# Kernel tuning notes

Hardware: AMD Instinct MI355X
Metric: run time of the kernel (lower is better)

## Reference

```python
import jax, jax.numpy as jnp
import numpy as np

N, D, M, H, FF, L = 8192, 14, 36, 256, 2048, 2  # rows, d_model, material feats, mlp hidden, ffn, layers
EPS = 1e-5


def _ln(x, g, b):
    mu = jnp.mean(x, axis=-1, keepdims=True)
    var = jnp.mean((x - mu) ** 2, axis=-1, keepdims=True)
    return (x - mu) * jax.lax.rsqrt(var + EPS) * g + b


def setup_inputs() -> dict:
    key = jax.random.key(0)
    ks = iter(jax.random.split(key, 32))
    p = lambda shape, fan: jax.random.normal(next(ks), shape, jnp.float32) * (fan ** -0.5)
    return {
        "x": jax.random.normal(next(ks), (N, D), jnp.float32),
        "y": jax.random.normal(next(ks), (N, M), jnp.float32),
        # 2 post-LN TransformerEncoderLayers (nhead=1, dim_feedforward=2048, relu)
        "attn_wqkv": p((L, 3 * D, D), D), "attn_bqkv": p((L, 3 * D), D),
        "attn_wo": p((L, D, D), D), "attn_bo": p((L, D), D),
        "ln1_g": jnp.ones((L, D)), "ln1_b": jnp.zeros((L, D)),
        "ff_w1": p((L, FF, D), D), "ff_b1": p((L, FF), D),
        "ff_w2": p((L, D, FF), FF), "ff_b2": p((L, D), FF),
        "ln2_g": jnp.ones((L, D)), "ln2_b": jnp.zeros((L, D)),
        "fc1_w": p((D, D), D), "fc1_b": p((D,), D),
        "fc2_w": p((1, D), D), "fc2_b": p((1,), D),
        "fc3_w": p((H, D + M + 1), D + M + 1), "fc3_b": p((H,), D + M + 1),
        "fc4_w": p((H, H), H), "fc4_b": p((H,), H),
        "fc5_w": p((1, H), H), "fc5_b": p((1,), H),
    }


def reference(x, y, attn_wqkv, attn_bqkv, attn_wo, attn_bo, ln1_g, ln1_b,
              ff_w1, ff_b1, ff_w2, ff_b2, ln2_g, ln2_b,
              fc1_w, fc1_b, fc2_w, fc2_b, fc3_w, fc3_b, fc4_w, fc4_b, fc5_w, fc5_b):
    h = x  # [N, D]; batch of size 1 squeezed away
    for l in range(L):
        qkv = h @ attn_wqkv[l].T + attn_bqkv[l]            # [N, 3D]
        q, k, v = jnp.split(qkv, 3, axis=-1)
        scores = (q @ k.T) * (D ** -0.5)                   # [N, N]
        a = jax.nn.softmax(scores, axis=-1) @ v            # [N, D]
        a = a @ attn_wo[l].T + attn_bo[l]
        h = _ln(h + a, ln1_g[l], ln1_b[l])
        f = jax.nn.relu(h @ ff_w1[l].T + ff_b1[l]) @ ff_w2[l].T + ff_b2[l]
        h = _ln(h + f, ln2_g[l], ln2_b[l])
    x1 = h @ fc1_w.T + fc1_b                               # [N, D]
    size_out = (x1 @ fc2_w.T + fc2_b)[:, 0]                # [N]

    # batched replacement of the per-row python loop
    size_int = size_out.astype(jnp.int32)                  # trunc toward zero, like .int()
    size_f = size_int.astype(jnp.float32)[:, None]         # [N, 1]
    reg_in = jnp.concatenate([size_f, x, y], axis=1)       # [N, 1+D+M]
    r = jax.nn.relu(reg_in @ fc3_w.T + fc3_b)
    r = jax.nn.relu(r @ fc4_w.T + fc4_b)
    reg_values = (r @ fc5_w.T + fc5_b)[:, 0]               # [N]
    reg_values = jnp.where(size_int != 0, reg_values, 0.0)
    return size_out, reg_values
```

## Files before the change

### kernel.cpp

```cpp
#include <hip/hip_runtime.h>
#include <math.h>

#define NN 8192
#define DD 14
#define DP 16
#define FF 2048
#define HID 256
#define LN_EPS 1e-5f
#define NCH 16
#define NFCH 8
#define QSCALE (1.4426950408889634f / 3.7416573867739413f)

typedef short bf16x8 __attribute__((ext_vector_type(8)));
typedef float f32x4 __attribute__((ext_vector_type(4)));

#define LOAD16(dst, srcp) { \
  const float4* _p = (const float4*)(srcp); \
  float4 _a = _p[0], _b = _p[1], _c = _p[2], _d = _p[3]; \
  dst[0]=_a.x; dst[1]=_a.y; dst[2]=_a.z; dst[3]=_a.w; \
  dst[4]=_b.x; dst[5]=_b.y; dst[6]=_b.z; dst[7]=_b.w; \
  dst[8]=_c.x; dst[9]=_c.y; dst[10]=_c.z; dst[11]=_c.w; \
  dst[12]=_d.x; dst[13]=_d.y; dst[14]=_d.z; dst[15]=_d.w; }

#define STORE16(dstp, src) { \
  float4* _p = (float4*)(dstp); \
  _p[0] = make_float4(src[0], src[1], src[2], src[3]); \
  _p[1] = make_float4(src[4], src[5], src[6], src[7]); \
  _p[2] = make_float4(src[8], src[9], src[10], src[11]); \
  _p[3] = make_float4(src[12], src[13], src[14], src[15]); }

static __device__ __forceinline__ float fast_exp2(float x) {
#if __has_builtin(__builtin_amdgcn_exp2f)
  return __builtin_amdgcn_exp2f(x);
#else
  return exp2f(x);
#endif
}

static __device__ __forceinline__ unsigned short bf_hi(float x) {
  return (unsigned short)(__float_as_uint(x) >> 16);
}
static __device__ __forceinline__ float bf_hi_f(float x) {
  return __uint_as_float(__float_as_uint(x) & 0xffff0000u);
}

static __device__ __forceinline__ void split8(const float* pv, bf16x8* ph, bf16x8* pl) {
  #pragma unroll
  for (int i = 0; i < 8; i++) {
    unsigned int u = __float_as_uint(pv[i]);
    (*ph)[i] = (short)(u >> 16);
    float rr = pv[i] - __uint_as_float(u & 0xffff0000u);
    (*pl)[i] = (short)(__float_as_uint(rr) >> 16);
  }
}

static __device__ __forceinline__ void qkv_compute_store(
    int r, const float* hr, const float* __restrict__ wqkv,
    const float* __restrict__ bqkv, unsigned int* __restrict__ Qpack,
    unsigned int* __restrict__ KB1, unsigned int* __restrict__ KB2,
    unsigned short* __restrict__ VhiT, unsigned short* __restrict__ VloT) {
  float q[14], k[14], v[14];
  #pragma unroll 6
  for (int c = 0; c < 42; c++) {
    const float* w = wqkv + c * 14;
    float s = bqkv[c];
    #pragma unroll
    for (int d = 0; d < 14; d++) s = fmaf(hr[d], w[d], s);
    if (c < 14)       q[c] = s * QSCALE;
    else if (c < 28)  k[c - 14] = s;
    else              v[c - 28] = s;
  }
  unsigned int qp[16], k1[16], k2[16];
  unsigned short qh[14], ql[14], kh[14], kl[14];
  #pragma unroll
  for (int d = 0; d < 14; d++) {
    qh[d] = bf_hi(q[d]);
    ql[d] = bf_hi(q[d] - bf_hi_f(q[d]));
    kh[d] = bf_hi(k[d]);
    kl[d] = bf_hi(k[d] - bf_hi_f(k[d]));
  }
  #pragma unroll
  for (int i = 0; i < 7; i++) {
    qp[i]     = (unsigned int)qh[2*i] | ((unsigned int)qh[2*i+1] << 16);
    qp[8 + i] = (unsigned int)ql[2*i] | ((unsigned int)ql[2*i+1] << 16);
    k1[i]     = (unsigned int)kh[2*i] | ((unsigned int)kh[2*i+1] << 16);
    k1[8 + i] = k1[i];
    k2[i]     = (unsigned int)kl[2*i] | ((unsigned int)kl[2*i+1] << 16);
    k2[8 + i] = k2[i];
  }
  qp[7] = 0; qp[15] = 0; k1[7] = 0; k1[15] = 0; k2[7] = 0; k2[15] = 0;
  uint4* Qp4 = (uint4*)(Qpack + (size_t)r * 16);
  uint4* K14 = (uint4*)(KB1 + (size_t)r * 16);
  uint4* K24 = (uint4*)(KB2 + (size_t)r * 16);
  #pragma unroll
  for (int i = 0; i < 4; i++) {
    Qp4[i] = make_uint4(qp[4*i], qp[4*i+1], qp[4*i+2], qp[4*i+3]);
    K14[i] = make_uint4(k1[4*i], k1[4*i+1], k1[4*i+2], k1[4*i+3]);
    K24[i] = make_uint4(k2[4*i], k2[4*i+1], k2[4*i+2], k2[4*i+3]);
  }
  #pragma unroll
  for (int d = 0; d < 14; d++) {
    VhiT[(size_t)d * NN + r] = bf_hi(v[d]);
    VloT[(size_t)d * NN + r] = bf_hi(v[d] - bf_hi_f(v[d]));
  }
  VhiT[(size_t)14 * NN + r] = 0x3F80;
  VhiT[(size_t)15 * NN + r] = 0;
  VloT[(size_t)14 * NN + r] = 0;
  VloT[(size_t)15 * NN + r] = 0;
}

static __device__ __forceinline__ void store_apack(unsigned int* dst, const float* o) {
  unsigned int qp[16];
  unsigned short hh[14], ll[14];
  #pragma unroll
  for (int d = 0; d < 14; d++) {
    hh[d] = bf_hi(o[d]);
    ll[d] = bf_hi(o[d] - bf_hi_f(o[d]));
  }
  #pragma unroll
  for (int i = 0; i < 7; i++) {
    qp[i]     = (unsigned int)hh[2*i] | ((unsigned int)hh[2*i+1] << 16);
    qp[8 + i] = (unsigned int)ll[2*i] | ((unsigned int)ll[2*i+1] << 16);
  }
  qp[7] = 0; qp[15] = 0;
  uint4* d4 = (uint4*)dst;
  #pragma unroll
  for (int i = 0; i < 4; i++)
    d4[i] = make_uint4(qp[4*i], qp[4*i+1], qp[4*i+2], qp[4*i+3]);
}

__global__ void pack_all(const float* __restrict__ w3, const float* __restrict__ w4,
                         const float* __restrict__ ffw1, const float* __restrict__ ffw2,
                         const float* __restrict__ x, const float* __restrict__ wqkv,
                         const float* __restrict__ bqkv, float* __restrict__ h,
                         unsigned int* __restrict__ Qpack,
                         unsigned int* __restrict__ KB1, unsigned int* __restrict__ KB2,
                         unsigned short* __restrict__ VhiT, unsigned short* __restrict__ VloT,
                         unsigned short* __restrict__ B3h, unsigned short* __restrict__ B3l,
                         unsigned short* __restrict__ B4h, unsigned short* __restrict__ B4l,
                         unsigned int* __restrict__ W1B1, unsigned int* __restrict__ W1B2,
                         unsigned short* __restrict__ W2h, unsigned short* __restrict__ W2l) {
  const int blk = blockIdx.x, tid = threadIdx.x;
  if (blk < 32) {
    int t = blk * 256 + tid;
    int lane = t & 63, ks = (t >> 6) & 7, nt = t >> 9;
    int n = nt * 16 + (lane & 15);
    int k0 = ks * 32 + (lane >> 4) * 8;
    unsigned int h4[4], l4[4];
    #pragma unroll
    for (int jj = 0; jj < 4; jj++) {
      unsigned short h2[2], l2[2];
      #pragma unroll
      for (int e = 0; e < 2; e++) {
        float v = w4[(size_t)n * 256 + k0 + jj * 2 + e];
        h2[e] = bf_hi(v);
        l2[e] = bf_hi(v - bf_hi_f(v));
      }
      h4[jj] = (unsigned int)h2[0] | ((unsigned int)h2[1] << 16);
      l4[jj] = (unsigned int)l2[0] | ((unsigned int)l2[1] << 16);
    }
    ((uint4*)B4h)[t] = make_uint4(h4[0], h4[1], h4[2], h4[3]);
    ((uint4*)B4l)[t] = make_uint4(l4[0], l4[1], l4[2], l4[3]);
    if (ks < 2) {
      int fi = (nt * 2 + ks) * 64 + lane;
      #pragma unroll
      for (int jj = 0; jj < 4; jj++) {
        unsigned short h2[2], l2[2];
        #pragma unroll
        for (int e = 0; e < 2; e++) {
          int k = k0 + jj * 2 + e;
          float v = (k < 51) ? w3[(size_t)n * 51 + k] : 0.f;
          h2[e] = bf_hi(v);
          l2[e] = bf_hi(v - bf_hi_f(v));
        }
        h4[jj] = (unsigned int)h2[0] | ((unsigned int)h2[1] << 16);
        l4[jj] = (unsigned int)l2[0] | ((unsigned int)l2[1] << 16);
      }
      ((uint4*)B3h)[fi] = make_uint4(h4[0], h4[1], h4[2], h4[3]);
      ((uint4*)B3l)[fi] = make_uint4(l4[0], l4[1], l4[2], l4[3]);
    }
  } else if (blk < 48) {
    int t = (blk - 32) * 256 + tid;
    int l = t >> 11, j = t & 2047;
    const float* wrow = ffw1 + ((size_t)l * FF + j) * 14;
    unsigned int k1[16], k2[16];
    unsigned short kh[14], kl[14];
    #pragma unroll
    for (int d = 0; d < 14; d++) {
      float v = wrow[d];
      kh[d] = bf_hi(v);
      kl[d] = bf_hi(v - bf_hi_f(v));
    }
    #pragma unroll
    for (int i = 0; i < 7; i++) {
      k1[i] = (unsigned int)kh[2*i] | ((unsigned int)kh[2*i+1] << 16);
      k1[8 + i] = k1[i];
      k2[i] = (unsigned int)kl[2*i] | ((unsigned int)kl[2*i+1] << 16);
      k2[8 + i] = k2[i];
    }
    k1[7] = 0; k1[15] = 0; k2[7] = 0; k2[15] = 0;
    uint4* d1 = (uint4*)(W1B1 + (size_t)t * 16);
    uint4* d2 = (uint4*)(W1B2 + (size_t)t * 16);
    #pragma unroll
    for (int i = 0; i < 4; i++) {
      d1[i] = make_uint4(k1[4*i], k1[4*i+1], k1[4*i+2], k1[4*i+3]);
      d2[i] = make_uint4(k2[4*i], k2[4*i+1], k2[4*i+2], k2[4*i+3]);
    }
  } else if (blk < 64) {
    int t = (blk - 48) * 256 + tid;
    int l = t >> 11, j = t & 2047;
    #pragma unroll
    for (int d = 0; d < 16; d++) {
      float v = (d < 14) ? ffw2[((size_t)l * 14 + d) * FF + j] : 0.f;
      W2h[((size_t)l * 16 + d) * FF + j] = bf_hi(v);
      W2l[((size_t)l * 16 + d) * FF + j] = bf_hi(v - bf_hi_f(v));
    }
  } else {
    int r = (blk - 64) * 256 + tid;
    float hr[16];
    #pragma unroll
    for (int d = 0; d < 14; d++) hr[d] = x[(size_t)r * 14 + d];
    hr[14] = 0.f; hr[15] = 0.f;
    STORE16(h + (size_t)r * DP, hr);
    qkv_compute_store(r, hr, wqkv, bqkv, Qpack, KB1, KB2, VhiT, VloT);
  }
}

__global__ __launch_bounds__(256, 4) void attn_mfma(
    const unsigned int* __restrict__ Qpack, const unsigned int* __restrict__ KB1,
    const unsigned int* __restrict__ KB2, const unsigned short* __restrict__ VhiT,
    const unsigned short* __restrict__ VloT, float* __restrict__ part) {
  __shared__ float Plds[4][32][36];
  const int tid = threadIdx.x;
  const int wave = tid >> 6;
  const int lane = tid & 63;
  const int lo4 = lane & 15;
  const int hi4 = lane >> 4;
  const int qbase = blockIdx.x * 128 + wave * 32;
  const int kbase0 = blockIdx.y * 512;

  const bf16x8* Qp = (const bf16x8*)Qpack;
  const bf16x8* B1 = (const bf16x8*)KB1;
  const bf16x8* B2 = (const bf16x8*)KB2;
  const bf16x8* Vh = (const bf16x8*)VhiT;
  const bf16x8* Vl = (const bf16x8*)VloT;

  bf16x8 aQ0 = Qp[(size_t)(qbase + lo4) * 4 + hi4];
  bf16x8 aQ1 = Qp[(size_t)(qbase + 16 + lo4) * 4 + hi4];
  f32x4 acc0 = {0.f, 0.f, 0.f, 0.f};
  f32x4 acc1 = {0.f, 0.f, 0.f, 0.f};
  const f32x4 zero = {0.f, 0.f, 0.f, 0.f};

  for (int c = 0; c < 16; c++) {
    const int kb = kbase0 + c * 32;
    bf16x8 b1g0 = B1[(size_t)(kb + lo4) * 4 + hi4];
    bf16x8 b2g0 = B2[(size_t)(kb + lo4) * 4 + hi4];
    bf16x8 b1g1 = B1[(size_t)(kb + 16 + lo4) * 4 + hi4];
    bf16x8 b2g1 = B2[(size_t)(kb + 16 + lo4) * 4 + hi4];
    bf16x8 vh = Vh[(size_t)lo4 * 1024 + (kb >> 3) + hi4];
    bf16x8 vl = Vl[(size_t)lo4 * 1024 + (kb >> 3) + hi4];

    f32x4 s00 = __builtin_amdgcn_mfma_f32_16x16x32_bf16(aQ0, b1g0, zero, 0, 0, 0);
    f32x4 s01 = __builtin_amdgcn_mfma_f32_16x16x32_bf16(aQ0, b1g1, zero, 0, 0, 0);
    f32x4 s10 = __builtin_amdgcn_mfma_f32_16x16x32_bf16(aQ1, b1g0, zero, 0, 0, 0);
    f32x4 s11 = __builtin_amdgcn_mfma_f32_16x16x32_bf16(aQ1, b1g1, zero, 0, 0, 0);
    s00 = __builtin_amdgcn_mfma_f32_16x16x32_bf16(aQ0, b2g0, s00, 0, 0, 0);
    s01 = __builtin_amdgcn_mfma_f32_16x16x32_bf16(aQ0, b2g1, s01, 0, 0, 0);
    s10 = __builtin_amdgcn_mfma_f32_16x16x32_bf16(aQ1, b2g0, s10, 0, 0, 0);
    s11 = __builtin_amdgcn_mfma_f32_16x16x32_bf16(aQ1, b2g1, s11, 0, 0, 0);
    #pragma unroll
    for (int reg = 0; reg < 4; reg++) {
      Plds[wave][hi4 * 4 + reg][lo4]           = fast_exp2(s00[reg]);
      Plds[wave][hi4 * 4 + reg][16 + lo4]      = fast_exp2(s01[reg]);
      Plds[wave][16 + hi4 * 4 + reg][lo4]      = fast_exp2(s10[reg]);
      Plds[wave][16 + hi4 * 4 + reg][16 + lo4] = fast_exp2(s11[reg]);
    }
    __asm__ volatile("s_waitcnt lgkmcnt(0)" ::: "memory");
    const float4* p0 = (const float4*)&Plds[wave][lo4][hi4 * 8];
    const float4* p1 = (const float4*)&Plds[wave][16 + lo4][hi4 * 8];
    float4 a0 = p0[0], a1 = p0[1], c0 = p1[0], c1 = p1[1];
    float pv0[8] = {a0.x, a0.y, a0.z, a0.w, a1.x, a1.y, a1.z, a1.w};
    float pv1[8] = {c0.x, c0.y, c0.z, c0.w, c1.x, c1.y, c1.z, c1.w};
// ... 205 lines not shown
    const float* __restrict__ h, const float* __restrict__ part,
    const float* __restrict__ b2, const float* __restrict__ g, const float* __restrict__ b,
    const float* __restrict__ fc1w, const float* __restrict__ fc1b,
    const float* __restrict__ fc2w, const float* __restrict__ fc2b,
    const float* __restrict__ x, const float* __restrict__ y,
    const unsigned short* __restrict__ B3h, const unsigned short* __restrict__ B3l,
    const float* __restrict__ b3,
    const unsigned short* __restrict__ B4h, const unsigned short* __restrict__ B4l,
    const float* __restrict__ b4,
    const float* __restrict__ w5, const float* __restrict__ b5,
    float* __restrict__ out, float* __restrict__ outr) {
  __shared__ alignas(16) unsigned short Ah[16][72], Al[16][72];
  __shared__ alignas(16) unsigned short R1h[16][264], R1l[16][264];
  __shared__ float sred[4][16][16];
  __shared__ float szf[16];
  const int tid = threadIdx.x;
  const int wave = tid >> 6;
  const int lane = tid & 63;
  const int lo4 = lane & 15;
  const int hi4 = lane >> 4;
  const int rbase = blockIdx.x * 16;

  if (tid < 128) {
    int m = tid >> 3, c = tid & 7;
    int r = rbase + m;
    float p[16];
    LOAD16(p, part + ((size_t)c * NN + r) * 16);
    float f[14];
    #pragma unroll
    for (int d = 0; d < 14; d++) f[d] = p[d];
    #pragma unroll
    for (int off = 1; off < 8; off <<= 1) {
      #pragma unroll
      for (int d = 0; d < 14; d++) f[d] += __shfl_xor(f[d], off, 64);
    }
    if (c == 0) {
      float hr[16];
      LOAD16(hr, h + (size_t)r * DP);
      float xx[14];
      #pragma unroll
      for (int i = 0; i < 14; i++) xx[i] = hr[i] + f[i] + b2[i];
      float mu = 0.f;
      #pragma unroll
      for (int i = 0; i < 14; i++) mu += xx[i];
      mu *= (1.f / 14.f);
      float var = 0.f;
      #pragma unroll
      for (int i = 0; i < 14; i++) { float tt = xx[i] - mu; var = fmaf(tt, tt, var); }
      var *= (1.f / 14.f);
      float rs = rsqrtf(var + LN_EPS);
      float o[14];
      #pragma unroll
      for (int i = 0; i < 14; i++) o[i] = fmaf((xx[i] - mu) * rs, g[i], b[i]);
      float s = fc2b[0];
      #pragma unroll
      for (int i = 0; i < 14; i++) {
        float tt = fc1b[i];
        #pragma unroll
        for (int d = 0; d < 14; d++) tt = fmaf(fc1w[i * 14 + d], o[d], tt);
        s = fmaf(tt, fc2w[i], s);
      }
      out[r] = s;
      int si = (int)s;
      szf[m] = (float)si;
    }
  }
  __syncthreads();

  for (int idx = tid; idx < 16 * 64; idx += 256) {
    int m = idx >> 6, k = idx & 63;
    int r = rbase + m;
    float v = 0.f;
    if (k == 0)       v = szf[m];
    else if (k < 15)  v = x[(size_t)r * 14 + (k - 1)];
    else if (k < 51)  v = y[(size_t)r * 36 + (k - 15)];
    Ah[m][k] = bf_hi(v);
    Al[m][k] = bf_hi(v - bf_hi_f(v));
  }
  __syncthreads();

  const f32x4 zero = {0.f, 0.f, 0.f, 0.f};
  f32x4 acc[4];
  #pragma unroll
  for (int nt = 0; nt < 4; nt++) acc[nt] = zero;

  #pragma unroll
  for (int ks = 0; ks < 2; ks++) {
    bf16x8 ah = *(const bf16x8*)&Ah[lo4][ks * 32 + hi4 * 8];
    bf16x8 al = *(const bf16x8*)&Al[lo4][ks * 32 + hi4 * 8];
    #pragma unroll
    for (int nt = 0; nt < 4; nt++) {
      int fi = ((wave * 4 + nt) * 2 + ks) * 64 + lane;
      bf16x8 bh = ((const bf16x8*)B3h)[fi];
      bf16x8 bl = ((const bf16x8*)B3l)[fi];
      acc[nt] = __builtin_amdgcn_mfma_f32_16x16x32_bf16(ah, bh, acc[nt], 0, 0, 0);
      acc[nt] = __builtin_amdgcn_mfma_f32_16x16x32_bf16(al, bh, acc[nt], 0, 0, 0);
      acc[nt] = __builtin_amdgcn_mfma_f32_16x16x32_bf16(ah, bl, acc[nt], 0, 0, 0);
    }
  }
  #pragma unroll
  for (int nt = 0; nt < 4; nt++) {
    int n = (wave * 4 + nt) * 16 + lo4;
    float bb = b3[n];
    #pragma unroll
    for (int reg = 0; reg < 4; reg++) {
      int m = hi4 * 4 + reg;
      float v = fmaxf(acc[nt][reg] + bb, 0.f);
      R1h[m][n] = bf_hi(v);
      R1l[m][n] = bf_hi(v - bf_hi_f(v));
    }
  }
  __syncthreads();

  #pragma unroll
  for (int nt = 0; nt < 4; nt++) acc[nt] = zero;
  #pragma unroll
  for (int ks = 0; ks < 8; ks++) {
    bf16x8 ah = *(const bf16x8*)&R1h[lo4][ks * 32 + hi4 * 8];
    bf16x8 al = *(const bf16x8*)&R1l[lo4][ks * 32 + hi4 * 8];
    #pragma unroll
    for (int nt = 0; nt < 4; nt++) {
      int fi = ((wave * 4 + nt) * 8 + ks) * 64 + lane;
      bf16x8 bh = ((const bf16x8*)B4h)[fi];
      bf16x8 bl = ((const bf16x8*)B4l)[fi];
      acc[nt] = __builtin_amdgcn_mfma_f32_16x16x32_bf16(ah, bh, acc[nt], 0, 0, 0);
      acc[nt] = __builtin_amdgcn_mfma_f32_16x16x32_bf16(al, bh, acc[nt], 0, 0, 0);
      acc[nt] = __builtin_amdgcn_mfma_f32_16x16x32_bf16(ah, bl, acc[nt], 0, 0, 0);
    }
  }
  float s[4] = {0.f, 0.f, 0.f, 0.f};
  #pragma unroll
  for (int nt = 0; nt < 4; nt++) {
    int n = (wave * 4 + nt) * 16 + lo4;
    float bb = b4[n], ww = w5[n];
    #pragma unroll
    for (int reg = 0; reg < 4; reg++)
      s[reg] = fmaf(fmaxf(acc[nt][reg] + bb, 0.f), ww, s[reg]);
  }
  #pragma unroll
  for (int reg = 0; reg < 4; reg++) sred[wave][hi4 * 4 + reg][lo4] = s[reg];
  __syncthreads();

  if (tid < 16) {
    float t = b5[0];
    #pragma unroll
    for (int w = 0; w < 4; w++) {
      const float4* p = (const float4*)&sred[w][tid][0];
      float4 a0 = p[0], a1 = p[1], a2 = p[2], a3 = p[3];
      t += ((a0.x + a0.y) + (a0.z + a0.w)) + ((a1.x + a1.y) + (a1.z + a1.w)) +
           ((a2.x + a2.y) + (a2.z + a2.w)) + ((a3.x + a3.y) + (a3.z + a3.w));
    }
    float sz = szf[tid];
    outr[rbase + tid] = (sz != 0.f) ? t : 0.f;
  }
}

extern "C" void kernel_launch(void* const* d_in, const int* in_sizes, int n_in,
                              void* d_out, int out_size, void* d_ws, size_t ws_size,
                              hipStream_t stream) {
  const float* x    = (const float*)d_in[0];
  const float* y    = (const float*)d_in[1];
  const float* wqkv = (const float*)d_in[2];
  const float* bqkv = (const float*)d_in[3];
  const float* wo   = (const float*)d_in[4];
  const float* bo   = (const float*)d_in[5];
  const float* ln1g = (const float*)d_in[6];
  const float* ln1b = (const float*)d_in[7];
  const float* ffw1 = (const float*)d_in[8];
  const float* ffb1 = (const float*)d_in[9];
  const float* ffw2 = (const float*)d_in[10];
  const float* ffb2 = (const float*)d_in[11];
  const float* ln2g = (const float*)d_in[12];
  const float* ln2b = (const float*)d_in[13];
  const float* fc1w = (const float*)d_in[14];
  const float* fc1b = (const float*)d_in[15];
  const float* fc2w = (const float*)d_in[16];
  const float* fc2b = (const float*)d_in[17];
  const float* fc3w = (const float*)d_in[18];
  const float* fc3b = (const float*)d_in[19];
  const float* fc4w = (const float*)d_in[20];
  const float* fc4b = (const float*)d_in[21];
  const float* fc5w = (const float*)d_in[22];
  const float* fc5b = (const float*)d_in[23];

  float* ws = (float*)d_ws;
  float*          h     = ws;
  unsigned int*   Qpack = (unsigned int*)(ws + 131072);
  unsigned int*   KB1   = (unsigned int*)(ws + 262144);
  unsigned int*   KB2   = (unsigned int*)(ws + 393216);
  unsigned short* VhiT  = (unsigned short*)(ws + 524288);
  unsigned short* VloT  = (unsigned short*)(ws + 589824);
  unsigned int*   Hpack = (unsigned int*)(ws + 655360);
  float*          part  = ws + 786432;
  unsigned short* B3h   = (unsigned short*)(ws + 2891776);
  unsigned short* B3l   = (unsigned short*)(ws + 2899968);
  unsigned short* B4h   = (unsigned short*)(ws + 2908160);
  unsigned short* B4l   = (unsigned short*)(ws + 2940928);
  unsigned int*   W1B1  = (unsigned int*)(ws + 2973696);
  unsigned int*   W1B2  = (unsigned int*)(ws + 3039232);
  unsigned short* W2h   = (unsigned short*)(ws + 3104768);
  unsigned short* W2l   = (unsigned short*)(ws + 3137536);

  float* out = (float*)d_out;

  pack_all<<<96, 256, 0, stream>>>(fc3w, fc4w, ffw1, ffw2, x, wqkv, bqkv, h,
                                   Qpack, KB1, KB2, VhiT, VloT,
                                   B3h, B3l, B4h, B4l, W1B1, W1B2, W2h, W2l);
  for (int l = 0; l < 2; l++) {
    attn_mfma<<<dim3(64, NCH), 256, 0, stream>>>(Qpack, KB1, KB2, VhiT, VloT, part);
    attn_comb_ln1<<<256, 128, 0, stream>>>(h, part, wo + (size_t)l * 196,
                                           bo + (size_t)l * 14, ln1g + (size_t)l * 14,
                                           ln1b + (size_t)l * 14, Hpack);
    ffn_mfma<<<dim3(64, NFCH), 256, 0, stream>>>(
        Hpack, W1B1 + (size_t)l * 2048 * 16, W1B2 + (size_t)l * 2048 * 16,
        W2h + (size_t)l * 16 * FF, W2l + (size_t)l * 16 * FF,
        ffb1 + (size_t)l * FF, part);
    if (l == 0) {
      ffn_ln2_qkv<<<256, 128, 0, stream>>>(h, part, ffb2, ln2g, ln2b,
                                           wqkv + 42 * 14, bqkv + 42,
                                           Qpack, KB1, KB2, VhiT, VloT);
    }
  }
  tail_fused<<<512, 256, 0, stream>>>(h, part, ffb2 + 14, ln2g + 14, ln2b + 14,
                                      fc1w, fc1b, fc2w, fc2b, x, y,
                                      B3h, B3l, fc3b, B4h, B4l, fc4b,
                                      fc5w, fc5b, out, out + NN);
}
```

Baseline: 258.5 us.

## Fuse all pipeline stages into one persistent cooperative kernel with grid syncs

Replaces the sequence of nine kernel launches (packing, attention, combine+LN, FFN, LN+QKV, tail) with a single persistent cooperative kernel that loops over virtual blocks and separates stages with grid-wide syncs. The goal is to remove per-launch overhead and inter-kernel gaps on a short pipeline. In exchange, every stage runs at a fixed grid size capped by occupancy, and it pays grid.sync costs. If the cooperative launch fails, it falls back to the old multi-kernel path.

```diff
diff --git a/kernel.cpp b/kernel.cpp
--- a/kernel.cpp
+++ b/kernel.cpp
@@ -1,5 +1,8 @@
 #include <hip/hip_runtime.h>
+#include <hip/hip_cooperative_groups.h>
 #include <math.h>
+
+namespace cg = cooperative_groups;
 
 #define NN 8192
 #define DD 14
@@ -128,6 +131,7 @@
   for (int i = 0; i < 4; i++)
     d4[i] = make_uint4(qp[4*i], qp[4*i+1], qp[4*i+2], qp[4*i+3]);
 }
+
 
 __global__ void pack_all(const float* __restrict__ w3, const float* __restrict__ w4,
                          const float* __restrict__ ffw1, const float* __restrict__ ffw2,
@@ -639,6 +643,518 @@
     }
     float sz = szf[tid];
     outr[rbase + tid] = (sz != 0.f) ? t : 0.f;
+  }
+}
+
+
+struct P26 {
+  const float *x, *y, *wqkv, *bqkv, *wo, *bo, *ln1g, *ln1b;
+  const float *ffw1, *ffb1, *ffw2, *ffb2, *ln2g, *ln2b;
+  const float *fc1w, *fc1b, *fc2w, *fc2b, *fc3w, *fc3b, *fc4w, *fc4b, *fc5w, *fc5b;
+  float* ws;
+  float* out;
+};
+
+__global__ __launch_bounds__(256, 4) void fused_pipeline(P26 p) {
+  cg::grid_group grid = cg::this_grid();
+  __shared__ __attribute__((aligned(16))) char smem[25664];
+  const int tid = threadIdx.x;
+  const int wave = tid >> 6;
+  const int lane = tid & 63;
+  const int lo4 = lane & 15;
+  const int hi4 = lane >> 4;
+
+  float* ws = p.ws;
+  float*          h     = ws;
+  unsigned int*   Qpack = (unsigned int*)(ws + 131072);
+  unsigned int*   KB1   = (unsigned int*)(ws + 262144);
+  unsigned int*   KB2   = (unsigned int*)(ws + 393216);
+  unsigned short* VhiT  = (unsigned short*)(ws + 524288);
+  unsigned short* VloT  = (unsigned short*)(ws + 589824);
+  unsigned int*   Hpack = (unsigned int*)(ws + 655360);
+  float*          part  = ws + 786432;
+  unsigned short* B3h   = (unsigned short*)(ws + 2891776);
+  unsigned short* B3l   = (unsigned short*)(ws + 2899968);
+  unsigned short* B4h   = (unsigned short*)(ws + 2908160);
+  unsigned short* B4l   = (unsigned short*)(ws + 2940928);
+  unsigned int*   W1B1  = (unsigned int*)(ws + 2973696);
+  unsigned int*   W1B2  = (unsigned int*)(ws + 3039232);
+  unsigned short* W2h   = (unsigned short*)(ws + 3104768);
+  unsigned short* W2l   = (unsigned short*)(ws + 3137536);
+  float* out  = p.out;
+  float* outr = p.out + NN;
+
+  for (int vb = blockIdx.x; vb < 96; vb += gridDim.x) {
+    if (vb < 32) {
+      int t = vb * 256 + tid;
+      int ln = t & 63, ks = (t >> 6) & 7, nt = t >> 9;
+      int n = nt * 16 + (ln & 15);
+      int k0 = ks * 32 + (ln >> 4) * 8;
+      unsigned int h4[4], l4[4];
+      #pragma unroll
+      for (int jj = 0; jj < 4; jj++) {
+        unsigned short h2[2], l2[2];
+        #pragma unroll
+        for (int e = 0; e < 2; e++) {
+          float v = p.fc4w[(size_t)n * 256 + k0 + jj * 2 + e];
+          h2[e] = bf_hi(v);
+          l2[e] = bf_hi(v - bf_hi_f(v));
+        }
+        h4[jj] = (unsigned int)h2[0] | ((unsigned int)h2[1] << 16);
+        l4[jj] = (unsigned int)l2[0] | ((unsigned int)l2[1] << 16);
+      }
+      ((uint4*)B4h)[t] = make_uint4(h4[0], h4[1], h4[2], h4[3]);
+      ((uint4*)B4l)[t] = make_uint4(l4[0], l4[1], l4[2], l4[3]);
+      if (ks < 2) {
+        int fi = (nt * 2 + ks) * 64 + ln;
+        #pragma unroll
+        for (int jj = 0; jj < 4; jj++) {
+          unsigned short h2[2], l2[2];
+          #pragma unroll
+          for (int e = 0; e < 2; e++) {
+            int k = k0 + jj * 2 + e;
+            float v = (k < 51) ? p.fc3w[(size_t)n * 51 + k] : 0.f;
+            h2[e] = bf_hi(v);
+            l2[e] = bf_hi(v - bf_hi_f(v));
+          }
+          h4[jj] = (unsigned int)h2[0] | ((unsigned int)h2[1] << 16);
+          l4[jj] = (unsigned int)l2[0] | ((unsigned int)l2[1] << 16);
+        }
+        ((uint4*)B3h)[fi] = make_uint4(h4[0], h4[1], h4[2], h4[3]);
+        ((uint4*)B3l)[fi] = make_uint4(l4[0], l4[1], l4[2], l4[3]);
+      }
+    } else if (vb < 48) {
+      int t = (vb - 32) * 256 + tid;
+      int lw = t >> 11, j = t & 2047;
+      const float* wrow = p.ffw1 + ((size_t)lw * FF + j) * 14;
+      unsigned int k1[16], k2[16];
+      unsigned short kh[14], kl[14];
+      #pragma unroll
+      for (int d = 0; d < 14; d++) {
+        float v = wrow[d];
+        kh[d] = bf_hi(v);
+        kl[d] = bf_hi(v - bf_hi_f(v));
+      }
+      #pragma unroll
+      for (int i = 0; i < 7; i++) {
+        k1[i] = (unsigned int)kh[2*i] | ((unsigned int)kh[2*i+1] << 16);
+        k1[8 + i] = k1[i];
+        k2[i] = (unsigned int)kl[2*i] | ((unsigned int)kl[2*i+1] << 16);
+        k2[8 + i] = k2[i];
+      }
+      k1[7] = 0; k1[15] = 0; k2[7] = 0; k2[15] = 0;
+      uint4* d1 = (uint4*)(W1B1 + (size_t)t * 16);
+      uint4* d2 = (uint4*)(W1B2 + (size_t)t * 16);
+      #pragma unroll
+      for (int i = 0; i < 4; i++) {
+        d1[i] = make_uint4(k1[4*i], k1[4*i+1], k1[4*i+2], k1[4*i+3]);
+        d2[i] = make_uint4(k2[4*i], k2[4*i+1], k2[4*i+2], k2[4*i+3]);
+      }
+    } else if (vb < 64) {
+      int t = (vb - 48) * 256 + tid;
+      int lw = t >> 11, j = t & 2047;
+      #pragma unroll
+      for (int d = 0; d < 16; d++) {
+        float v = (d < 14) ? p.ffw2[((size_t)lw * 14 + d) * FF + j] : 0.f;
+        W2h[((size_t)lw * 16 + d) * FF + j] = bf_hi(v);
+        W2l[((size_t)lw * 16 + d) * FF + j] = bf_hi(v - bf_hi_f(v));
+      }
+    } else {
+      int r = (vb - 64) * 256 + tid;
+      float hr[16];
+      #pragma unroll
+      for (int d = 0; d < 14; d++) hr[d] = p.x[(size_t)r * 14 + d];
+      hr[14] = 0.f; hr[15] = 0.f;
+      STORE16(h + (size_t)r * DP, hr);
+      qkv_compute_store(r, hr, p.wqkv, p.bqkv, Qpack, KB1, KB2, VhiT, VloT);
+    }
+  }
+  grid.sync();
+
+  const bf16x8* Qp  = (const bf16x8*)Qpack;
+  const bf16x8* Kb1 = (const bf16x8*)KB1;
+  const bf16x8* Kb2 = (const bf16x8*)KB2;
+  const bf16x8* Vh  = (const bf16x8*)VhiT;
+  const bf16x8* Vl  = (const bf16x8*)VloT;
+  const bf16x8* Hp  = (const bf16x8*)Hpack;
+  const f32x4 zero = {0.f, 0.f, 0.f, 0.f};
+
+  for (int l = 0; l < 2; l++) {
+    for (int vb = blockIdx.x; vb < 1024; vb += gridDim.x) {
+      float (*Pl)[36] = reinterpret_cast<float(*)[36]>(smem + wave * 4608);
+      const int qbase = (vb & 63) * 128 + wave * 32;
+      const int kbase0 = (vb >> 6) * 512;
+      bf16x8 aQ0 = Qp[(size_t)(qbase + lo4) * 4 + hi4];
+      bf16x8 aQ1 = Qp[(size_t)(qbase + 16 + lo4) * 4 + hi4];
+      f32x4 acc0 = zero, acc1 = zero;
+      for (int c = 0; c < 16; c++) {
+        const int kb = kbase0 + c * 32;
+        bf16x8 b1g0 = Kb1[(size_t)(kb + lo4) * 4 + hi4];
+        bf16x8 b2g0 = Kb2[(size_t)(kb + lo4) * 4 + hi4];
+        bf16x8 b1g1 = Kb1[(size_t)(kb + 16 + lo4) * 4 + hi4];
+        bf16x8 b2g1 = Kb2[(size_t)(kb + 16 + lo4) * 4 + hi4];
+        bf16x8 vh = Vh[(size_t)lo4 * 1024 + (kb >> 3) + hi4];
+        bf16x8 vl = Vl[(size_t)lo4 * 1024 + (kb >> 3) + hi4];
+
+        f32x4 s00 = __builtin_amdgcn_mfma_f32_16x16x32_bf16(aQ0, b1g0, zero, 0, 0, 0);
+        f32x4 s01 = __builtin_amdgcn_mfma_f32_16x16x32_bf16(aQ0, b1g1, zero, 0, 0, 0);
+        f32x4 s10 = __builtin_amdgcn_mfma_f32_16x16x32_bf16(aQ1, b1g0, zero, 0, 0, 0);
+        f32x4 s11 = __builtin_amdgcn_mfma_f32_16x16x32_bf16(aQ1, b1g1, zero, 0, 0, 0);
+        s00 = __builtin_amdgcn_mfma_f32_16x16x32_bf16(aQ0, b2g0, s00, 0, 0, 0);
+        s01 = __builtin_amdgcn_mfma_f32_16x16x32_bf16(aQ0, b2g1, s01, 0, 0, 0);
+        s10 = __builtin_amdgcn_mfma_f32_16x16x32_bf16(aQ1, b2g0, s10, 0, 0, 0);
+        s11 = __builtin_amdgcn_mfma_f32_16x16x32_bf16(aQ1, b2g1, s11, 0, 0, 0);
+        #pragma unroll
+        for (int reg = 0; reg < 4; reg++) {
+          Pl[hi4 * 4 + reg][lo4]           = fast_exp2(s00[reg]);
+          Pl[hi4 * 4 + reg][16 + lo4]      = fast_exp2(s01[reg]);
+          Pl[16 + hi4 * 4 + reg][lo4]      = fast_exp2(s10[reg]);
+          Pl[16 + hi4 * 4 + reg][16 + lo4] = fast_exp2(s11[reg]);
+        }
+        __asm__ volatile("s_waitcnt lgkmcnt(0)" ::: "memory");
+        const float4* p0 = (const float4*)&Pl[lo4][hi4 * 8];
+        const float4* p1 = (const float4*)&Pl[16 + lo4][hi4 * 8];
+        float4 a0 = p0[0], a1 = p0[1], c0 = p1[0], c1 = p1[1];
+        float pv0[8] = {a0.x, a0.y, a0.z, a0.w, a1.x, a1.y, a1.z, a1.w};
+        float pv1[8] = {c0.x, c0.y, c0.z, c0.w, c1.x, c1.y, c1.z, c1.w};
+        bf16x8 ph0, pl0, ph1, pl1;
+        split8(pv0, &ph0, &pl0);
+        split8(pv1, &ph1, &pl1);
+        acc0 = __builtin_amdgcn_mfma_f32_16x16x32_bf16(ph0, vh, acc0, 0, 0, 0);
+        acc1 = __builtin_amdgcn_mfma_f32_16x16x32_bf16(ph1, vh, acc1, 0, 0, 0);
+        acc0 = __builtin_amdgcn_mfma_f32_16x16x32_bf16(pl0, vh, acc0, 0, 0, 0);
+        acc1 = __builtin_amdgcn_mfma_f32_16x16x32_bf16(pl1, vh, acc1, 0, 0, 0);
+        acc0 = __builtin_amdgcn_mfma_f32_16x16x32_bf16(ph0, vl, acc0, 0, 0, 0);
+        acc1 = __builtin_amdgcn_mfma_f32_16x16x32_bf16(ph1, vl, acc1, 0, 0, 0);
+        __asm__ volatile("s_waitcnt lgkmcnt(0)" ::: "memory");
+      }
+      float* pbase = part + (size_t)(vb >> 6) * NN * 16;
+      #pragma unroll
+      for (int reg = 0; reg < 4; reg++) {
+        int row0 = qbase + hi4 * 4 + reg;
+        pbase[(size_t)row0 * 16 + lo4] = acc0[reg];
+        pbase[(size_t)(row0 + 16) * 16 + lo4] = acc1[reg];
+      }
+    }
+    grid.sync();
+
+    {
+      const float* wol = p.wo + (size_t)l * 196;
+      const float* bol = p.bo + (size_t)l * 14;
+      const float* g1  = p.ln1g + (size_t)l * 14;
+      const float* bl1 = p.ln1b + (size_t)l * 14;
+      for (int vb = blockIdx.x; vb < 1024; vb += gridDim.x) {
+        int t = vb * 256 + tid;
+        int r = t >> 5, q = t & 31;
+        float L = 0.f;
+        float A[14];
+        #pragma unroll
+        for (int d = 0; d < 14; d++) A[d] = 0.f;
+        if (q < 16) {
+          float pp[16];
+          LOAD16(pp, part + ((size_t)q * NN + r) * 16);
+          L = pp[14];
+          #pragma unroll
+          for (int d = 0; d < 14; d++) A[d] = pp[d];
+        }
+        #pragma unroll
+        for (int off = 1; off < 16; off <<= 1) {
+          L += __shfl_xor(L, off, 64);
+          #pragma unroll
+          for (int d = 0; d < 14; d++) A[d] += __shfl_xor(A[d], off, 64);
+        }
+        if (q == 0) {
+          float inv = 1.f / L;
+          float a[14];
+          #pragma unroll
+          for (int d = 0; d < 14; d++) a[d] = A[d] * inv;
+          float hr[16];
+          LOAD16(hr, h + (size_t)r * DP);
+          float xx[14];
+          #pragma unroll
+          for (int i = 0; i < 14; i++) {
+            float s = bol[i];
+            #pragma unroll
+            for (int d = 0; d < 14; d++) s = fmaf(wol[i * 14 + d], a[d], s);
+            xx[i] = hr[i] + s;
+          }
+          float mu = 0.f;
+          #pragma unroll
+          for (int i = 0; i < 14; i++) mu += xx[i];
+          mu *= (1.f / 14.f);
+          float var = 0.f;
+          #pragma unroll
+          for (int i = 0; i < 14; i++) { float tt = xx[i] - mu; var = fmaf(tt, tt, var); }
+          var *= (1.f / 14.f);
+          float rs = rsqrtf(var + LN_EPS);
+          float o[16];
+          #pragma unroll
+          for (int i = 0; i < 14; i++) o[i] = fmaf((xx[i] - mu) * rs, g1[i], bl1[i]);
+          o[14] = 0.f; o[15] = 0.f;
+          STORE16(h + (size_t)r * DP, o);
+          store_apack(Hpack + (size_t)r * 16, o);
+        }
+      }
+    }
+    grid.sync();
+
+    {
+      const bf16x8* Wb1 = (const bf16x8*)(W1B1 + (size_t)l * 2048 * 16);
+      const bf16x8* Wb2 = (const bf16x8*)(W1B2 + (size_t)l * 2048 * 16);
+      const bf16x8* Wvh = (const bf16x8*)(W2h + (size_t)l * 16 * FF);
+      const bf16x8* Wvl = (const bf16x8*)(W2l + (size_t)l * 16 * FF);
+      const float* fb1 = p.ffb1 + (size_t)l * FF;
+      for (int vb = blockIdx.x; vb < 1024; vb += gridDim.x) {
+        float (*Pl)[36] = reinterpret_cast<float(*)[36]>(smem + wave * 4608);
+        const int qbase = (vb & 63) * 128 + wave * 32;
+        const int jbase0 = (vb >> 6) * 128;
+        bf16x8 aH0 = Hp[(size_t)(qbase + lo4) * 4 + hi4];
+        bf16x8 aH1 = Hp[(size_t)(qbase + 16 + lo4) * 4 + hi4];
+        f32x4 acc0 = zero, acc1 = zero;
+        for (int c = 0; c < 4; c++) {
+          const int jb = jbase0 + c * 32;
+          bf16x8 b1g0 = Wb1[(size_t)(jb + lo4) * 4 + hi4];
+          bf16x8 b2g0 = Wb2[(size_t)(jb + lo4) * 4 + hi4];
+          bf16x8 b1g1 = Wb1[(size_t)(jb + 16 + lo4) * 4 + hi4];
+          bf16x8 b2g1 = Wb2[(size_t)(jb + 16 + lo4) * 4 + hi4];
+          bf16x8 vh = Wvh[(size_t)lo4 * 256 + (jb >> 3) + hi4];
+          bf16x8 vl = Wvl[(size_t)lo4 * 256 + (jb >> 3) + hi4];
+          float bb0 = fb1[jb + lo4];
+          float bb1 = fb1[jb + 16 + lo4];
+
+          f32x4 s00 = __builtin_amdgcn_mfma_f32_16x16x32_bf16(aH0, b1g0, zero, 0, 0, 0);
+          f32x4 s01 = __builtin_amdgcn_mfma_f32_16x16x32_bf16(aH0, b1g1, zero, 0, 0, 0);
+          f32x4 s10 = __builtin_amdgcn_mfma_f32_16x16x32_bf16(aH1, b1g0, zero, 0, 0, 0);
+          f32x4 s11 = __builtin_amdgcn_mfma_f32_16x16x32_bf16(aH1, b1g1, zero, 0, 0, 0);
+          s00 = __builtin_amdgcn_mfma_f32_16x16x32_bf16(aH0, b2g0, s00, 0, 0, 0);
+          s01 = __builtin_amdgcn_mfma_f32_16x16x32_bf16(aH0, b2g1, s01, 0, 0, 0);
+          s10 = __builtin_amdgcn_mfma_f32_16x16x32_bf16(aH1, b2g0, s10, 0, 0, 0);
+          s11 = __builtin_amdgcn_mfma_f32_16x16x32_bf16(aH1, b2g1, s11, 0, 0, 0);
+          #pragma unroll
+          for (int reg = 0; reg < 4; reg++) {
+            Pl[hi4 * 4 + reg][lo4]           = fmaxf(s00[reg] + bb0, 0.f);
+            Pl[hi4 * 4 + reg][16 + lo4]      = fmaxf(s01[reg] + bb1, 0.f);
+            Pl[16 + hi4 * 4 + reg][lo4]      = fmaxf(s10[reg] + bb0, 0.f);
+            Pl[16 + hi4 * 4 + reg][16 + lo4] = fmaxf(s11[reg] + bb1, 0.f);
+          }
+          __asm__ volatile("s_waitcnt lgkmcnt(0)" ::: "memory");
+          const float4* p0 = (const float4*)&Pl[lo4][hi4 * 8];
+          const float4* p1 = (const float4*)&Pl[16 + lo4][hi4 * 8];
+          float4 a0 = p0[0], a1 = p0[1], c0 = p1[0], c1 = p1[1];
+          float pv0[8] = {a0.x, a0.y, a0.z, a0.w, a1.x, a1.y, a1.z, a1.w};
+          float pv1[8] = {c0.x, c0.y, c0.z, c0.w, c1.x, c1.y, c1.z, c1.w};
+          bf16x8 th0, tl0, th1, tl1;
+          split8(pv0, &th0, &tl0);
+          split8(pv1, &th1, &tl1);
+          acc0 = __builtin_amdgcn_mfma_f32_16x16x32_bf16(th0, vh, acc0, 0, 0, 0);
+          acc1 = __builtin_amdgcn_mfma_f32_16x16x32_bf16(th1, vh, acc1, 0, 0, 0);
+          acc0 = __builtin_amdgcn_mfma_f32_16x16x32_bf16(tl0, vh, acc0, 0, 0, 0);
+          acc1 = __builtin_amdgcn_mfma_f32_16x16x32_bf16(tl1, vh, acc1, 0, 0, 0);
+          acc0 = __builtin_amdgcn_mfma_f32_16x16x32_bf16(th0, vl, acc0, 0, 0, 0);
+          acc1 = __builtin_amdgcn_mfma_f32_16x16x32_bf16(th1, vl, acc1, 0, 0, 0);
+          __asm__ volatile("s_waitcnt lgkmcnt(0)" ::: "memory");
+        }
+        float* pbase = part + (size_t)(vb >> 6) * NN * 16;
+        #pragma unroll
+        for (int reg = 0; reg < 4; reg++) {
+          int row0 = qbase + hi4 * 4 + reg;
+          pbase[(size_t)row0 * 16 + lo4] = acc0[reg];
+          pbase[(size_t)(row0 + 16) * 16 + lo4] = acc1[reg];
+        }
+      }
+    }
+    grid.sync();
+
+    if (l == 0) {
+      for (int vb = blockIdx.x; vb < 1024; vb += gridDim.x) {
+        int t = vb * 256 + tid;
+        int r = t >> 5, q = t & 31;
+        float f[14];
+        #pragma unroll
+        for (int d = 0; d < 14; d++) f[d] = 0.f;
+        if (q < 16) {
+          float pp[16];
+          LOAD16(pp, part + ((size_t)q * NN + r) * 16);
+          #pragma unroll
+          for (int d = 0; d < 14; d++) f[d] = pp[d];
+        }
+        #pragma unroll
+        for (int off = 1; off < 16; off <<= 1) {
+          #pragma unroll
+          for (int d = 0; d < 14; d++) f[d] += __shfl_xor(f[d], off, 64);
+        }
+        if (q == 0) {
+          float hr[16];
+          LOAD16(hr, h + (size_t)r * DP);
+          float xx[14];
+          #pragma unroll
+          for (int i = 0; i < 14; i++) xx[i] = hr[i] + f[i] + p.ffb2[i];
+          float mu = 0.f;
+          #pragma unroll
+          for (int i = 0; i < 14; i++) mu += xx[i];
+          mu *= (1.f / 14.f);
+          float var = 0.f;
+          #pragma unroll
+          for (int i = 0; i < 14; i++) { float tt = xx[i] - mu; var = fmaf(tt, tt, var); }
+          var *= (1.f / 14.f);
+          float rs = rsqrtf(var + LN_EPS);
+          float o[16];
+          #pragma unroll
+          for (int i = 0; i < 14; i++) o[i] = fmaf((xx[i] - mu) * rs, p.ln2g[i], p.ln2b[i]);
+          o[14] = 0.f; o[15] = 0.f;
+          STORE16(h + (size_t)r * DP, o);
+          qkv_compute_store(r, o, p.wqkv + 588, p.bqkv + 42, Qpack, KB1, KB2, VhiT, VloT);
+        }
+      }
+      grid.sync();
+    }
+  }
+
+  {
+    unsigned short (*Ah)[72]  = (unsigned short(*)[72])(smem);
+    unsigned short (*Al)[72]  = (unsigned short(*)[72])(smem + 2304);
+    unsigned short (*R1h)[264] = (unsigned short(*)[264])(smem + 4608);
+    unsigned short (*R1l)[264] = (unsigned short(*)[264])(smem + 13056);
+    float (*sred)[16][16] = (float(*)[16][16])(smem + 21504);
+    float* szf = (float*)(smem + 25600);
+    const float* b2t = p.ffb2 + 14;
+    const float* g2t = p.ln2g + 14;
+    const float* bb2t = p.ln2b + 14;
+
+    for (int vb = blockIdx.x; vb < 512; vb += gridDim.x) {
+      const int rbase = vb * 16;
+      {
+        int m = tid >> 4, c = tid & 15;
+        int r = rbase + m;
+        float pp[16];
+        LOAD16(pp, part + ((size_t)c * NN + r) * 16);
+        float f[14];
+        #pragma unroll
+        for (int d = 0; d < 14; d++) f[d] = pp[d];
+        #pragma unroll
+        for (int off = 1; off < 16; off <<= 1) {
+          #pragma unroll
+          for (int d = 0; d < 14; d++) f[d] += __shfl_xor(f[d], off, 64);
+        }
+        if (c == 0) {
+          float hr[16];
+          LOAD16(hr, h + (size_t)r * DP);
+          float xx[14];
+          #pragma unroll
+          for (int i = 0; i < 14; i++) xx[i] = hr[i] + f[i] + b2t[i];
+          float mu = 0.f;
+          #pragma unroll
+          for (int i = 0; i < 14; i++) mu += xx[i];
+          mu *= (1.f / 14.f);
+          float var = 0.f;
+          #pragma unroll
+          for (int i = 0; i < 14; i++) { float tt = xx[i] - mu; var = fmaf(tt, tt, var); }
+          var *= (1.f / 14.f);
+          float rs = rsqrtf(var + LN_EPS);
+          float o[14];
+          #pragma unroll
+          for (int i = 0; i < 14; i++) o[i] = fmaf((xx[i] - mu) * rs, g2t[i], bb2t[i]);
+          float s = p.fc2b[0];
+          #pragma unroll
+          for (int i = 0; i < 14; i++) {
+            float tt = p.fc1b[i];
+            #pragma unroll
+            for (int d = 0; d < 14; d++) tt = fmaf(p.fc1w[i * 14 + d], o[d], tt);
+            s = fmaf(tt, p.fc2w[i], s);
+          }
+          out[r] = s;
+          int si = (int)s;
+          szf[m] = (float)si;
+        }
+      }
+      __syncthreads();
+
+      for (int idx = tid; idx < 16 * 64; idx += 256) {
+        int m = idx >> 6, k = idx & 63;
+        int r = rbase + m;
+        float v = 0.f;
+        if (k == 0)       v = szf[m];
+        else if (k < 15)  v = p.x[(size_t)r * 14 + (k - 1)];
+        else if (k < 51)  v = p.y[(size_t)r * 36 + (k - 15)];
+        Ah[m][k] = bf_hi(v);
+        Al[m][k] = bf_hi(v - bf_hi_f(v));
+      }
+      __syncthreads();
+
+      f32x4 acc[4];
+      #pragma unroll
+      for (int nt = 0; nt < 4; nt++) acc[nt] = zero;
+      #pragma unroll
+      for (int ks = 0; ks < 2; ks++) {
+        bf16x8 ah = *(const bf16x8*)&Ah[lo4][ks * 32 + hi4 * 8];
+        bf16x8 al = *(const bf16x8*)&Al[lo4][ks * 32 + hi4 * 8];
+        #pragma unroll
+        for (int nt = 0; nt < 4; nt++) {
+          int fi = ((wave * 4 + nt) * 2 + ks) * 64 + lane;
+          bf16x8 bh = ((const bf16x8*)B3h)[fi];
+          bf16x8 bl = ((const bf16x8*)B3l)[fi];
+          acc[nt] = __builtin_amdgcn_mfma_f32_16x16x32_bf16(ah, bh, acc[nt], 0, 0, 0);
+          acc[nt] = __builtin_amdgcn_mfma_f32_16x16x32_bf16(al, bh, acc[nt], 0, 0, 0);
+          acc[nt] = __builtin_amdgcn_mfma_f32_16x16x32_bf16(ah, bl, acc[nt], 0, 0, 0);
+        }
+      }
+      #pragma unroll
+      for (int nt = 0; nt < 4; nt++) {
+        int n = (wave * 4 + nt) * 16 + lo4;
+        float bb = p.fc3b[n];
+        #pragma unroll
+        for (int reg = 0; reg < 4; reg++) {
+          int m = hi4 * 4 + reg;
+          float v = fmaxf(acc[nt][reg] + bb, 0.f);
+          R1h[m][n] = bf_hi(v);
+          R1l[m][n] = bf_hi(v - bf_hi_f(v));
+        }
+      }
+      __syncthreads();
+
+      #pragma unroll
+      for (int nt = 0; nt < 4; nt++) acc[nt] = zero;
+      #pragma unroll
+      for (int ks = 0; ks < 8; ks++) {
+        bf16x8 ah = *(const bf16x8*)&R1h[lo4][ks * 32 + hi4 * 8];
+        bf16x8 al = *(const bf16x8*)&R1l[lo4][ks * 32 + hi4 * 8];
+        #pragma unroll
+        for (int nt = 0; nt < 4; nt++) {
+          int fi = ((wave * 4 + nt) * 8 + ks) * 64 + lane;
+          bf16x8 bh = ((const bf16x8*)B4h)[fi];
+          bf16x8 bl = ((const bf16x8*)B4l)[fi];
+          acc[nt] = __builtin_amdgcn_mfma_f32_16x16x32_bf16(ah, bh, acc[nt], 0, 0, 0);
+          acc[nt] = __builtin_amdgcn_mfma_f32_16x16x32_bf16(al, bh, acc[nt], 0, 0, 0);
+          acc[nt] = __builtin_amdgcn_mfma_f32_16x16x32_bf16(ah, bl, acc[nt], 0, 0, 0);
+        }
+      }
+      float s4[4] = {0.f, 0.f, 0.f, 0.f};
+      #pragma unroll
+      for (int nt = 0; nt < 4; nt++) {
+        int n = (wave * 4 + nt) * 16 + lo4;
+        float bb = p.fc4b[n], ww = p.fc5w[n];
+        #pragma unroll
+        for (int reg = 0; reg < 4; reg++)
+          s4[reg] = fmaf(fmaxf(acc[nt][reg] + bb, 0.f), ww, s4[reg]);
+      }
+      #pragma unroll
+      for (int reg = 0; reg < 4; reg++) sred[wave][hi4 * 4 + reg][lo4] = s4[reg];
+      __syncthreads();
+
+      if (tid < 16) {
+        float tsum = p.fc5b[0];
+        #pragma unroll
+        for (int w = 0; w < 4; w++) {
+          const float4* pr = (const float4*)&sred[w][tid][0];
+          float4 a0 = pr[0], a1 = pr[1], a2 = pr[2], a3 = pr[3];
+          tsum += ((a0.x + a0.y) + (a0.z + a0.w)) + ((a1.x + a1.y) + (a1.z + a1.w)) +
+                  ((a2.x + a2.y) + (a2.z + a2.w)) + ((a3.x + a3.y) + (a3.z + a3.w));
+        }
+        float sz = szf[tid];
+        outr[rbase + tid] = (sz != 0.f) ? tsum : 0.f;
+      }
+      __syncthreads();
+    }
   }
 }
 
@@ -690,26 +1206,53 @@
 
   float* out = (float*)d_out;
 
-  pack_all<<<96, 256, 0, stream>>>(fc3w, fc4w, ffw1, ffw2, x, wqkv, bqkv, h,
-                                   Qpack, KB1, KB2, VhiT, VloT,
-                                   B3h, B3l, B4h, B4l, W1B1, W1B2, W2h, W2l);
-  for (int l = 0; l < 2; l++) {
-    attn_mfma<<<dim3(64, NCH), 256, 0, stream>>>(Qpack, KB1, KB2, VhiT, VloT, part);
-    attn_comb_ln1<<<256, 128, 0, stream>>>(h, part, wo + (size_t)l * 196,
-                                           bo + (size_t)l * 14, ln1g + (size_t)l * 14,
-                                           ln1b + (size_t)l * 14, Hpack);
-    ffn_mfma<<<dim3(64, NFCH), 256, 0, stream>>>(
-        Hpack, W1B1 + (size_t)l * 2048 * 16, W1B2 + (size_t)l * 2048 * 16,
-        W2h + (size_t)l * 16 * FF, W2l + (size_t)l * 16 * FF,
-        ffb1 + (size_t)l * FF, part);
-    if (l == 0) {
-      ffn_ln2_qkv<<<256, 128, 0, stream>>>(h, part, ffb2, ln2g, ln2b,
-                                           wqkv + 42 * 14, bqkv + 42,
-                                           Qpack, KB1, KB2, VhiT, VloT);
-    }
-  }
-  tail_fused<<<512, 256, 0, stream>>>(h, part, ffb2 + 14, ln2g + 14, ln2b + 14,
-                                      fc1w, fc1b, fc2w, fc2b, x, y,
-                                      B3h, B3l, fc3b, B4h, B4l, fc4b,
-                                      fc5w, fc5b, out, out + NN);
-}
+  P26 hp;
+  hp.x = x; hp.y = y; hp.wqkv = wqkv; hp.bqkv = bqkv; hp.wo = wo; hp.bo = bo;
+  hp.ln1g = ln1g; hp.ln1b = ln1b; hp.ffw1 = ffw1; hp.ffb1 = ffb1;
+  hp.ffw2 = ffw2; hp.ffb2 = ffb2; hp.ln2g = ln2g; hp.ln2b = ln2b;
+  hp.fc1w = fc1w; hp.fc1b = fc1b; hp.fc2w = fc2w; hp.fc2b = fc2b;
+  hp.fc3w = fc3w; hp.fc3b = fc3b; hp.fc4w = fc4w; hp.fc4b = fc4b;
+  hp.fc5w = fc5w; hp.fc5b = fc5b;
+  hp.ws = ws; hp.out = out;
+
+  static int nblk = 0;
+  if (nblk == 0) {
+    int dev = 0, numCU = 0, perCU = 0;
+    (void)hipGetDevice(&dev);
+    (void)hipDeviceGetAttribute(&numCU, hipDeviceAttributeMultiprocessorCount, dev);
+    (void)hipOccupancyMaxActiveBlocksPerMultiprocessor(&perCU, fused_pipeline, 256, 0);
+    if (numCU <= 0) numCU = 256;
+    if (perCU <= 0) perCU = 1;
+    long cap = (long)perCU * (long)numCU;
+    nblk = (int)(cap < 1024 ? cap : 1024);
+  }
+
+  void* kargs[] = { (void*)&hp };
+  hipError_t err = hipLaunchCooperativeKernel(fused_pipeline, dim3(nblk), dim3(256),
+                                              kargs, 0, stream);
+  if (err != hipSuccess) {
+    (void)hipGetLastError();
+    pack_all<<<96, 256, 0, stream>>>(fc3w, fc4w, ffw1, ffw2, x, wqkv, bqkv, h,
+                                     Qpack, KB1, KB2, VhiT, VloT,
+                                     B3h, B3l, B4h, B4l, W1B1, W1B2, W2h, W2l);
+    for (int l = 0; l < 2; l++) {
+      attn_mfma<<<dim3(64, NCH), 256, 0, stream>>>(Qpack, KB1, KB2, VhiT, VloT, part);
+      attn_comb_ln1<<<256, 128, 0, stream>>>(h, part, wo + (size_t)l * 196,
+                                             bo + (size_t)l * 14, ln1g + (size_t)l * 14,
+                                             ln1b + (size_t)l * 14, Hpack);
+      ffn_mfma<<<dim3(64, NFCH), 256, 0, stream>>>(
+          Hpack, W1B1 + (size_t)l * 2048 * 16, W1B2 + (size_t)l * 2048 * 16,
+          W2h + (size_t)l * 16 * FF, W2l + (size_t)l * 16 * FF,
+          ffb1 + (size_t)l * FF, part);
+      if (l == 0) {
+        ffn_ln2_qkv<<<256, 128, 0, stream>>>(h, part, ffb2, ln2g, ln2b,
+                                             wqkv + 42 * 14, bqkv + 42,
+                                             Qpack, KB1, KB2, VhiT, VloT);
+      }
+    }
+    tail_fused<<<512, 256, 0, stream>>>(h, part, ffb2 + 14, ln2g + 14, ln2b + 14,
+                                        fc1w, fc1b, fc2w, fc2b, x, y,
+                                        B3h, B3l, fc3b, B4h, B4l, fc4b,
+                                        fc5w, fc5b, out, out + NN);
+  }
+}
```

After: 878.2 us. +239.7%, slower.
